# Performance work log

Measured on AMD Instinct MI355X. Metric: run time of the kernel, lower is better.

The kernel has to match this reference:

```python
import jax, jax.numpy as jnp
import numpy as np

D_MODEL, D_K, D_V, H, D_FF = 512, 64, 64, 8, 2048
B, N = 8, 1024
LN_EPS = 1e-5


def _layer_norm(x, g, b):
    mu = jnp.mean(x, axis=-1, keepdims=True)
    var = jnp.mean((x - mu) ** 2, axis=-1, keepdims=True)
    return (x - mu) * jax.lax.rsqrt(var + LN_EPS) * g + b


def setup_inputs() -> dict:
    key = jax.random.key(0)
    ks = jax.random.split(key, 16)
    s = 0.02
    return {
        "queries": jax.random.normal(ks[0], (B, N, D_MODEL), jnp.float32),
        "keys": jax.random.normal(ks[1], (B, N, D_MODEL), jnp.float32),
        "values": jax.random.normal(ks[2], (B, N, D_MODEL), jnp.float32),
        "relative_geometry_weights": jax.random.uniform(ks[3], (B, H, N, N), jnp.float32),
        "pos": jax.random.normal(ks[4], (B, N, D_MODEL), jnp.float32),
        "Wq": jax.random.normal(ks[5], (D_MODEL, H * D_K), jnp.float32) * s,
        "bq": jnp.zeros((H * D_K,), jnp.float32),
        "Wk": jax.random.normal(ks[6], (D_MODEL, H * D_K), jnp.float32) * s,
        "bk": jnp.zeros((H * D_K,), jnp.float32),
        "Wv": jax.random.normal(ks[7], (D_MODEL, H * D_V), jnp.float32) * s,
        "bv": jnp.zeros((H * D_V,), jnp.float32),
        "Wo": jax.random.normal(ks[8], (H * D_V, D_MODEL), jnp.float32) * s,
        "bo": jnp.zeros((D_MODEL,), jnp.float32),
        "ln1_g": jnp.ones((D_MODEL,), jnp.float32),
        "ln1_b": jnp.zeros((D_MODEL,), jnp.float32),
        "W1": jax.random.normal(ks[9], (D_MODEL, D_FF), jnp.float32) * s,
        "b1": jnp.zeros((D_FF,), jnp.float32),
        "W2": jax.random.normal(ks[10], (D_FF, D_MODEL), jnp.float32) * s,
        "b2": jnp.zeros((D_MODEL,), jnp.float32),
        "ln2_g": jnp.ones((D_MODEL,), jnp.float32),
        "ln2_b": jnp.zeros((D_MODEL,), jnp.float32),
    }


def reference(queries, keys, values, relative_geometry_weights, pos,
              Wq, bq, Wk, bk, Wv, bv, Wo, bo, ln1_g, ln1_b,
              W1, b1, W2, b2, ln2_g, ln2_b):
    b, n, _ = queries.shape
    # positional injection on q/k only
    q_in = queries + pos
    k_in = keys + pos
    # projections -> [b, h, n, d]
    q = (q_in @ Wq + bq).reshape(b, n, H, D_K).transpose(0, 2, 1, 3)
    k = (k_in @ Wk + bk).reshape(b, n, H, D_K).transpose(0, 2, 1, 3)
    v = (values @ Wv + bv).reshape(b, n, H, D_V).transpose(0, 2, 1, 3)
    # scaled dot-product scores with geometry bias: log(clamp(w_g)) + scores
    att = jnp.einsum('bhqd,bhkd->bhqk', q, k) / jnp.sqrt(jnp.float32(D_K))
    w_mn = jnp.log(jnp.clip(relative_geometry_weights, 1e-6, None)) + att
    w_mn = jax.nn.softmax(w_mn, axis=-1)
    out = jnp.einsum('bhqk,bhkd->bhqd', w_mn, v)  # [b,h,n,d_v]
    out = out.transpose(0, 2, 1, 3).reshape(b, n, H * D_V) @ Wo + bo
    # residual + layernorm (dropout is identity in eval)
    att_out = _layer_norm(queries + out, ln1_g, ln1_b)
    # position-wise FFN with residual + layernorm
    ff = jax.nn.relu(att_out @ W1 + b1) @ W2 + b2
    return _layer_norm(att_out + ff, ln2_g, ln2_b)
```

## Files before the change

### kernel.cpp

```cpp
#include <hip/hip_runtime.h>
#include <hip/hip_bf16.h>
#include <stdint.h>

#define B_   8
#define N_   1024
#define DM   512
#define H_   8
#define DFF  2048
#define ROWS (B_ * N_)
#define QKV_LD (3 * DM)
#define LOG2E 1.4426950408889634f
#define SCL  (0.125f * LOG2E)

typedef __bf16 bf16x8 __attribute__((ext_vector_type(8)));
typedef float  f32x4  __attribute__((ext_vector_type(4)));

__device__ __forceinline__ void gld_lds16(const void* g, void* l) {
  __builtin_amdgcn_global_load_lds((__attribute__((address_space(1))) void*)g,
                                   (__attribute__((address_space(3))) void*)l, 16, 0, 0);
}

__device__ __forceinline__ unsigned short bfb(float x) {
  __bf16 h = (__bf16)x;
  unsigned short u;
  __builtin_memcpy(&u, &h, 2);
  return u;
}

__global__ __launch_bounds__(256) void prep_and_wt(
    const float* __restrict__ q, const float* __restrict__ k,
    const float* __restrict__ v, const float* __restrict__ pos,
    __bf16* __restrict__ xq, __bf16* __restrict__ xk, __bf16* __restrict__ xv,
    const float* __restrict__ Wq, const float* __restrict__ Wk,
    const float* __restrict__ Wv, const float* __restrict__ Wo,
    const float* __restrict__ W1, const float* __restrict__ W2,
    __bf16* __restrict__ WqkvT, __bf16* __restrict__ WoT,
    __bf16* __restrict__ W1T, __bf16* __restrict__ W2T) {
  __shared__ float tl[32][33];
  if (blockIdx.x < 4096) {
    int i = blockIdx.x * 256 + threadIdx.x;
    float4 pv = ((const float4*)pos)[i];
    float4 qv = ((const float4*)q)[i];
    float4 kv = ((const float4*)k)[i];
    float4 vv = ((const float4*)v)[i];
    ushort4 o;
    o.x = bfb(qv.x + pv.x); o.y = bfb(qv.y + pv.y); o.z = bfb(qv.z + pv.z); o.w = bfb(qv.w + pv.w);
    ((ushort4*)xq)[i] = o;
    o.x = bfb(kv.x + pv.x); o.y = bfb(kv.y + pv.y); o.z = bfb(kv.z + pv.z); o.w = bfb(kv.w + pv.w);
    ((ushort4*)xk)[i] = o;
    o.x = bfb(vv.x); o.y = bfb(vv.y); o.z = bfb(vv.z); o.w = bfb(vv.w);
    ((ushort4*)xv)[i] = o;
    return;
  }
  int idx = blockIdx.x - 4096;
  const float* src; __bf16* dst; int K, N, t;
  if (idx < 768) {
    src = idx < 256 ? Wq : (idx < 512 ? Wk : Wv);
    dst = WqkvT + (size_t)(idx >> 8) * 512 * 512;
    K = 512; N = 512; t = idx & 255;
  } else if (idx < 1024) { src = Wo; dst = WoT;  K = 512;  N = 512;  t = idx - 768; }
  else if (idx < 2048)   { src = W1; dst = W1T;  K = 512;  N = 2048; t = idx - 1024; }
  else                   { src = W2; dst = W2T;  K = 2048; N = 512;  t = idx - 2048; }
  int tiles_n = N >> 5;
  int tn = t & (tiles_n - 1), tk = t / tiles_n;
  int n0 = tn * 32, k0 = tk * 32;
  int x = threadIdx.x & 31, y4 = threadIdx.x >> 5;
  #pragma unroll
  for (int j = y4; j < 32; j += 8) tl[j][x] = src[(size_t)(k0 + j) * N + n0 + x];
  __syncthreads();
  #pragma unroll
  for (int j = y4; j < 32; j += 8)
    dst[(size_t)(n0 + j) * K + k0 + x] = (__bf16)tl[x][j];
}

template <int EPI, int BN>
__global__ __launch_bounds__(256, 2) void gemm_bt(
    const __bf16* __restrict__ A0, const __bf16* __restrict__ A1, const __bf16* __restrict__ A2,
    const __bf16* __restrict__ BT,
    const float* __restrict__ bias0, const float* __restrict__ bias1, const float* __restrict__ bias2,
    void* __restrict__ Cp, __bf16* __restrict__ Vtp, int M, int N, int K, int nsplit) {
  constexpr int NFR = BN / 32;
  constexpr int WCW = BN / 2;
  constexpr int BI  = BN / 32;
  __shared__ __align__(16) __bf16 As[2][128 * 64];
  __shared__ __align__(16) __bf16 Bs[2][BN * 64];
  int tid = threadIdx.x, lane = tid & 63;
  int wave = tid >> 6;
  int wr = (wave >> 1) * 64, wc = (wave & 1) * WCW;

  int gx = N / BN;
  int nwg = gridDim.x;
  int cpx = nwg >> 3;
  int swz = (blockIdx.x & 7) * cpx + (blockIdx.x >> 3);
  int bx = swz % gx, by = swz / gx;
  int row0 = by << 7, col0 = bx * BN;

  int asel = col0 / nsplit;
  const __bf16* A = asel == 0 ? A0 : (asel == 1 ? A1 : A2);
  const float* bias = asel == 0 ? bias0 : (asel == 1 ? bias1 : bias2);

  f32x4 acc[4][NFR] = {};

#define GSTAGE(BUF, KT)                                                        \
  { _Pragma("unroll")                                                          \
    for (int i = 0; i < 4; ++i) {                                              \
      int t = i * 256 + tid;                                                   \
      int r = t >> 3, cS = (t & 7) ^ (r & 7);                                  \
      gld_lds16(A + (size_t)(row0 + r) * K + (KT) + cS * 8, As[BUF] + t * 8);  \
    }                                                                          \
    _Pragma("unroll")                                                          \
    for (int i = 0; i < BI; ++i) {                                             \
      int t = i * 256 + tid;                                                   \
      int r = t >> 3, cS = (t & 7) ^ (r & 7);                                  \
      gld_lds16(BT + (size_t)(col0 + r) * K + (KT) + cS * 8, Bs[BUF] + t * 8); \
    } }

#define GCOMP(BUF)                                                             \
  { const __bf16* Asc = As[BUF];                                               \
    const __bf16* Bsc = Bs[BUF];                                               \
    _Pragma("unroll")                                                          \
    for (int ks = 0; ks < 2; ++ks) {                                           \
      bf16x8 af[4], bfr[NFR];                                                  \
      _Pragma("unroll")                                                        \
      for (int m = 0; m < 4; ++m) {                                            \
        int r = wr + m * 16 + (lane & 15);                                     \
        int c = (ks * 4 + (lane >> 4)) ^ (r & 7);                              \
        af[m] = *(const bf16x8*)(Asc + r * 64 + c * 8);                        \
      }                                                                        \
      _Pragma("unroll")                                                        \
      for (int n = 0; n < NFR; ++n) {                                          \
        int r = wc + n * 16 + (lane & 15);                                     \
        int c = (ks * 4 + (lane >> 4)) ^ (r & 7);                              \
        bfr[n] = *(const bf16x8*)(Bsc + r * 64 + c * 8);                       \
      }                                                                        \
      _Pragma("unroll")                                                        \
      for (int m = 0; m < 4; ++m)                                              \
        _Pragma("unroll")                                                      \
        for (int n = 0; n < NFR; ++n)                                          \
          acc[m][n] = __builtin_amdgcn_mfma_f32_16x16x32_bf16(af[m], bfr[n], acc[m][n], 0, 0, 0); \
    } }

  GSTAGE(0, 0)
  int cur = 0;
  for (int kt = 64; kt < K; kt += 64) {
    GSTAGE(cur ^ 1, kt)
    if constexpr (BN == 128) asm volatile("s_waitcnt vmcnt(8)" ::: "memory");
    else                     asm volatile("s_waitcnt vmcnt(6)" ::: "memory");
    __builtin_amdgcn_s_barrier();
    __builtin_amdgcn_sched_barrier(0);
    GCOMP(cur)
    __builtin_amdgcn_s_barrier();
    cur ^= 1;
  }
  asm volatile("s_waitcnt vmcnt(0)" ::: "memory");
  __builtin_amdgcn_s_barrier();
  __builtin_amdgcn_sched_barrier(0);
  GCOMP(cur)
#undef GSTAGE
#undef GCOMP

  int rb = row0 + wr + ((lane >> 4) << 2);
  int cb = col0 + wc + (lane & 15);
  if (EPI == 3 && asel == 2) {
    int bb = row0 >> 10;
    #pragma unroll
    for (int n = 0; n < NFR; ++n) {
      int c = cb + n * 16;
      int d = c & 63, hh = (c >> 6) & 7;
      float bv = bias[c % nsplit];
      size_t vbase = ((size_t)((bb * 8 + hh) * 64 + d)) << 10;
      #pragma unroll
      for (int m = 0; m < 4; ++m) {
        int r0 = (rb + m * 16) & 1023;
        ushort4 pk;
        pk.x = bfb(acc[m][n][0] + bv);
        pk.y = bfb(acc[m][n][1] + bv);
        pk.z = bfb(acc[m][n][2] + bv);
        pk.w = bfb(acc[m][n][3] + bv);
        *(ushort4*)((__bf16*)Vtp + vbase + r0) = pk;
      }
    }
    return;
  }
  #pragma unroll
  for (int n = 0; n < NFR; ++n) {
    int c = cb + n * 16;
    float bv = bias[c % nsplit];
    #pragma unroll
    for (int m = 0; m < 4; ++m) {
      #pragma unroll
      for (int j = 0; j < 4; ++j) {
        int r = rb + m * 16 + j;
        float v = acc[m][n][j] + bv;
        if (EPI == 1) v = fmaxf(v, 0.f);
        if (EPI == 2) ((float*)Cp)[(size_t)r * N + c] = v;
        else          ((__bf16*)Cp)[(size_t)r * N + c] = (__bf16)v;
      }
    }
  }
}

__global__ __launch_bounds__(256, 4) void attn_kernel(
    const __bf16* __restrict__ QKV, const __bf16* __restrict__ Vt,
    const float* __restrict__ rgw, __bf16* __restrict__ O) {
  __shared__ __align__(16) __bf16 QsPs[64 * 64];
  __shared__ __align__(16) __bf16 Ks[2][64 * 64];
  __shared__ __align__(16) __bf16 Vs[2][64 * 64];

  int tid = threadIdx.x, lane = tid & 63, wave = tid >> 6;
  int flat = (blockIdx.x & 7) * 128 + (blockIdx.x >> 3);
  int qt = flat & 15, h = (flat >> 4) & 7, b = flat >> 7;
  int q0 = qt * 64;
  const int g = lane >> 4, u = lane & 15;

  const float* rgw_p = rgw +
      ((size_t)(b * H_ + h) * N_ + (size_t)(q0 + wave * 16 + u)) * N_ + g * 4;

#define STAGE_KV(BUF, KT)                                                      \
  {                                                                            \
    _Pragma("unroll")                                                          \
    for (int i = 0; i < 2; ++i) {                                              \
      int t = i * 256 + tid;                                                   \
      int r = t >> 3, cS = (t & 7) ^ (r & 7);                                  \
      gld_lds16(QKV + (size_t)(b * N_ + (KT) + r) * QKV_LD + DM + h * 64 + cS * 8, Ks[BUF] + t * 8); \
      gld_lds16(Vt + (size_t)((b * H_ + h) * 64 + r) * N_ + (KT) + cS * 8, Vs[BUF] + t * 8);         \
    }                                                                          \
  }
#define RPF(W, T)                                                              \
  {                                                                            \
    _Pragma("unroll")                                                          \
    for (int n = 0; n < 4; ++n)                                                \
      W[n] = __builtin_nontemporal_load((const f32x4*)(rgw_p + (size_t)(T) * 64 + n * 16)); \
  }

  #pragma unroll
  for (int i = 0; i < 2; ++i) {
    int t = i * 256 + tid;
    int r = t >> 3, cS = (t & 7) ^ (r & 7);
    gld_lds16(QKV + (size_t)(b * N_ + q0 + r) * QKV_LD + h * 64 + cS * 8, QsPs + t * 8);
  }
  STAGE_KV(0, 0)
  __builtin_amdgcn_sched_barrier(0);
  f32x4 wA[4], wB[4];
  RPF(wA, 0) RPF(wB, 1)
  __builtin_amdgcn_sched_barrier(0);

  float l = 0.f;
  f32x4 oacc[4] = {};
  bf16x8 qf[2];
  __bf16* pw = &QsPs[wave * 16 * 64];
  const int wrow = wave * 16 + u;
  union Pk { __bf16 h4[4]; unsigned long long q; };

#define PHASE(T16, WAITSTR, DOSTAGE, DORPF, WCON)                              \
  {                                                                            \
    asm volatile(WAITSTR ::: "memory");                                        \
    __builtin_amdgcn_s_barrier();                                              \
    if (DOSTAGE) { STAGE_KV(((T16) + 1) & 1, ((T16) + 1) * 64) }               \
    __builtin_amdgcn_sched_barrier(0);                                         \
    if ((T16) == 0) {                                                          \
      _Pragma("unroll")                                                        \
      for (int ks = 0; ks < 2; ++ks) {                                         \
        int c = (ks * 4 + g) ^ (wrow & 7);                                     \
        qf[ks] = *(const bf16x8*)(QsPs + wrow * 64 + c * 8);                   \
      }                                                                        \
    }                                                                          \
    f32x4 s[4] = {};                                                           \
    __builtin_amdgcn_s_setprio(1);                                             \
    _Pragma("unroll")                                                          \
    for (int ks = 0; ks < 2; ++ks) {                                           \
      _Pragma("unroll")                                                        \
      for (int n = 0; n < 4; ++n) {                                            \
        int r = n * 16 + u;                                                    \
        int c = (ks * 4 + g) ^ (r & 7);                                        \
        bf16x8 kf = *(const bf16x8*)(Ks[(T16) & 1] + r * 64 + c * 8);          \
        s[n] = __builtin_amdgcn_mfma_f32_16x16x32_bf16(kf, qf[ks], s[n], 0, 0, 0); \
      }                                                                        \
    }                                                                          \
    __builtin_amdgcn_s_setprio(0);                                             \
    if ((T16) == 0) __builtin_amdgcn_s_barrier();   \
    _Pragma("unroll")                                                          \
    for (int n = 0; n < 4; ++n) {                                              \
      Pk pk;                                                                   \
      _Pragma("unroll")                                                        \
      for (int j = 0; j < 4; ++j) {                                            \
        float pv = fmaxf(WCON[n][j], 1e-6f) * exp2f(s[n][j] * SCL);            \
        l += pv;                                                               \
        pk.h4[j] = (__bf16)pv;                                                 \
      }                                                                        \
      int bcol = 2 * n + (g >> 1);                                             \
      *(unsigned long long*)(pw + u * 64 + ((bcol ^ (u & 7)) << 3) + ((g & 1) << 2)) = pk.q; \
    }                                                                          \
    __builtin_amdgcn_sched_barrier(0);                                         \
    if (DORPF) { RPF(WCON, (T16) + 2) }                                        \
    __builtin_amdgcn_sched_barrier(0);                                         \
    __builtin_amdgcn_s_setprio(1);                                             \
    _Pragma("unroll")                                                          \
    for (int ks = 0; ks < 2; ++ks) {                                           \
      int cp = (ks * 4 + g) ^ (u & 7);                                         \
      bf16x8 pa = *(const bf16x8*)(pw + u * 64 + cp * 8);                      \
      _Pragma("unroll")                                                        \
      for (int n = 0; n < 4; ++n) {                                            \
        int r = n * 16 + u;                                                    \
        int c = (ks * 4 + g) ^ (r & 7);                                        \
        bf16x8 vb = *(const bf16x8*)(Vs[(T16) & 1] + r * 64 + c * 8);          \
        oacc[n] = __builtin_amdgcn_mfma_f32_16x16x32_bf16(pa, vb, oacc[n], 0, 0, 0); \
      }                                                                        \
    }                                                                          \
    __builtin_amdgcn_s_setprio(0);                                             \
  }

  PHASE(0,  "s_waitcnt vmcnt(8)", 1, 1, wA)
  PHASE(1,  "s_waitcnt vmcnt(4)", 1, 1, wB)
  PHASE(2,  "s_waitcnt vmcnt(4)", 1, 1, wA)
  PHASE(3,  "s_waitcnt vmcnt(4)", 1, 1, wB)
  PHASE(4,  "s_waitcnt vmcnt(4)", 1, 1, wA)
  PHASE(5,  "s_waitcnt vmcnt(4)", 1, 1, wB)
  PHASE(6,  "s_waitcnt vmcnt(4)", 1, 1, wA)
  PHASE(7,  "s_waitcnt vmcnt(4)", 1, 1, wB)
  PHASE(8,  "s_waitcnt vmcnt(4)", 1, 1, wA)
  PHASE(9,  "s_waitcnt vmcnt(4)", 1, 1, wB)
  PHASE(10, "s_waitcnt vmcnt(4)", 1, 1, wA)
  PHASE(11, "s_waitcnt vmcnt(4)", 1, 1, wB)
  PHASE(12, "s_waitcnt vmcnt(4)", 1, 1, wA)
  PHASE(13, "s_waitcnt vmcnt(4)", 1, 1, wB)
  PHASE(14, "s_waitcnt vmcnt(4)", 1, 0, wA)
  PHASE(15, "s_waitcnt vmcnt(0)", 0, 0, wB)
#undef PHASE
#undef STAGE_KV
#undef RPF

  l += __shfl_xor(l, 16);
  l += __shfl_xor(l, 32);
  float linv[4];
  #pragma unroll
  for (int j = 0; j < 4; ++j)
    linv[j] = 1.f / __shfl(l, (lane & 48) | (g * 4 + j));

  int orow = b * N_ + q0 + wave * 16 + g * 4;
  int ocol = h * 64 + u;
  #pragma unroll
  for (int j = 0; j < 4; ++j)
    #pragma unroll
    for (int n = 0; n < 4; ++n)
      O[(size_t)(orow + j) * DM + ocol + n * 16] = (__bf16)(oacc[n][j] * linv[j]);
}

template <int WRITE_BF, int X2BF>
__global__ __launch_bounds__(256) void ln_kernel(
    const float* __restrict__ x1, const void* __restrict__ x2v,
    const float* __restrict__ gw, const float* __restrict__ bw,
    float* __restrict__ outf, __bf16* __restrict__ outb) {
  __shared__ float red[8];
  int row = blockIdx.x, t = threadIdx.x;
  size_t base = (size_t)row * DM;
  float2 a = ((const float2*)(x1 + base))[t];
  float b0, b1;
  if (X2BF) {
    unsigned p = ((const unsigned*)x2v)[base / 2 + t];
    union { unsigned u; float f; } c0, c1;
    c0.u = p << 16; c1.u = p & 0xffff0000u;
    b0 = c0.f; b1 = c1.f;
  } else {
    float2 bb = ((const float2*)x2v)[base / 2 + t];
    b0 = bb.x; b1 = bb.y;
  }
  float v0 = a.x + b0, v1 = a.y + b1;
  float s = v0 + v1, s2 = v0 * v0 + v1 * v1;
  #pragma unroll
  for (int o = 32; o; o >>= 1) { s += __shfl_xor(s, o); s2 += __shfl_xor(s2, o); }
  int wave = t >> 6;
  if ((t & 63) == 0) { red[wave] = s; red[4 + wave] = s2; }
  __syncthreads();
  s = red[0] + red[1] + red[2] + red[3];
  s2 = red[4] + red[5] + red[6] + red[7];
  float mu = s * (1.f / DM);
  float var = s2 * (1.f / DM) - mu * mu;
  float rstd = rsqrtf(var + 1e-5f);
  float y0 = (v0 - mu) * rstd * gw[2 * t] + bw[2 * t];
  float y1 = (v1 - mu) * rstd * gw[2 * t + 1] + bw[2 * t + 1];
  float2 r; r.x = y0; r.y = y1;
  ((float2*)(outf + base))[t] = r;
  if (WRITE_BF) {
    ushort2 h; h.x = bfb(y0); h.y = bfb(y1);
    ((ushort2*)(outb + base))[t] = h;
  }
}

extern "C" void kernel_launch(void* const* d_in, const int* in_sizes, int n_in,
                              void* d_out, int out_size, void* d_ws, size_t ws_size,
                              hipStream_t stream) {
  const float* queries = (const float*)d_in[0];
  const float* keys    = (const float*)d_in[1];
  const float* values  = (const float*)d_in[2];
  const float* rgw     = (const float*)d_in[3];
  const float* pos     = (const float*)d_in[4];
  const float* Wq = (const float*)d_in[5];
  const float* bq = (const float*)d_in[6];
  const float* Wk = (const float*)d_in[7];
  const float* bk = (const float*)d_in[8];
  const float* Wv = (const float*)d_in[9];
  const float* bv = (const float*)d_in[10];
  const float* Wo = (const float*)d_in[11];
  const float* bo = (const float*)d_in[12];
  const float* ln1g = (const float*)d_in[13];
  const float* ln1b = (const float*)d_in[14];
  const float* W1 = (const float*)d_in[15];
  const float* b1 = (const float*)d_in[16];
  const float* W2 = (const float*)d_in[17];
  const float* b2 = (const float*)d_in[18];
  const float* ln2g = (const float*)d_in[19];
  const float* ln2b = (const float*)d_in[20];
  float* out = (float*)d_out;

  char* ws = (char*)d_ws;
  const size_t SZX = (size_t)ROWS * DM * 2;
  __bf16* Xq    = (__bf16*)(ws);
  __bf16* Xk    = (__bf16*)(ws + SZX);
  __bf16* Xv    = (__bf16*)(ws + 2 * SZX);
  __bf16* WqkvT = (__bf16*)(ws + 3 * SZX);
  __bf16* WoT   = (__bf16*)(ws + 3 * SZX + 1572864);
  __bf16* W1T   = (__bf16*)(ws + 3 * SZX + 2097152);
  __bf16* W2T   = (__bf16*)(ws + 3 * SZX + 4194304);
  __bf16* QKV   = (__bf16*)(ws + 3 * SZX + 6291456);
  __bf16* Vt    = (__bf16*)(ws + 3 * SZX + 6291456 + 3 * SZX);
  __bf16* Oat   = (__bf16*)(ws + 3 * SZX + 6291456 + 4 * SZX);
  __bf16* attprojb = Xq;
  __bf16* attoutb  = Xv;
  float*  attoutf  = (float*)QKV;
  __bf16* ff2b     = Vt;
  __bf16* ff1      = (__bf16*)(ws + 3 * SZX + 6291456 + 5 * SZX);

  prep_and_wt<<<4096 + 3072, 256, 0, stream>>>(
      queries, keys, values, pos, Xq, Xk, Xv,
      Wq, Wk, Wv, Wo, W1, W2, WqkvT, WoT, W1T, W2T);

  gemm_bt<3, 128><<<(ROWS / 128) * (QKV_LD / 128), 256, 0, stream>>>(
      Xq, Xk, Xv, WqkvT, bq, bk, bv, QKV, Vt, ROWS, QKV_LD, DM, DM);

  attn_kernel<<<B_ * H_ * (N_ / 64), 256, 0, stream>>>(QKV, Vt, rgw, Oat);

  gemm_bt<0, 64><<<(ROWS / 128) * (DM / 64), 256, 0, stream>>>(
      Oat, Oat, Oat, WoT, bo, bo, bo, attprojb, nullptr, ROWS, DM, DM, DM);

  ln_kernel<1, 1><<<ROWS, 256, 0, stream>>>(queries, attprojb, ln1g, ln1b, attoutf, attoutb);

  gemm_bt<1, 128><<<(ROWS / 128) * (DFF / 128), 256, 0, stream>>>(
      attoutb, attoutb, attoutb, W1T, b1, b1, b1, ff1, nullptr, ROWS, DFF, DM, DFF);

  gemm_bt<0, 64><<<(ROWS / 128) * (DM / 64), 256, 0, stream>>>(
      ff1, ff1, ff1, W2T, b2, b2, b2, ff2b, nullptr, ROWS, DM, DFF, DM);

  ln_kernel<0, 1><<<ROWS, 256, 0, stream>>>(attoutf, ff2b, ln2g, ln2b, out, nullptr);
}
```

Baseline: 209.8 us.

## Prefetch geometry weights in 128-column pairs and retune attention pipeline

Changes the attention kernel's geometry-weight prefetch from per-tile 64-column loads to 128-column loads covering two KV tiles. The loads are issued earlier in each even phase, and the vmcnt waits are restructured around the new schedule. It also swaps nontemporal loads for regular loads and lowers the launch-bounds occupancy hint from 4 to 3 to make room for the doubled register buffers (16 f32x4 instead of 8). The aim is deeper, longer-lived prefetch that hides the latency of the large rgw stream. The cost is more register pressure, fewer waves per CU, and a full vmcnt(0) drain every other phase.

```diff
diff --git a/kernel.cpp b/kernel.cpp
--- a/kernel.cpp
+++ b/kernel.cpp
@@ -200,7 +200,7 @@
   }
 }
 
-__global__ __launch_bounds__(256, 4) void attn_kernel(
+__global__ __launch_bounds__(256, 3) void attn_kernel(
     const __bf16* __restrict__ QKV, const __bf16* __restrict__ Vt,
     const float* __restrict__ rgw, __bf16* __restrict__ O) {
   __shared__ __align__(16) __bf16 QsPs[64 * 64];
@@ -226,11 +226,11 @@
       gld_lds16(Vt + (size_t)((b * H_ + h) * 64 + r) * N_ + (KT) + cS * 8, Vs[BUF] + t * 8);         \
     }                                                                          \
   }
-#define RPF(W, T)                                                              \
+#define RPF8(W, PQ)                                                            \
   {                                                                            \
     _Pragma("unroll")                                                          \
-    for (int n = 0; n < 4; ++n)                                                \
-      W[n] = __builtin_nontemporal_load((const f32x4*)(rgw_p + (size_t)(T) * 64 + n * 16)); \
+    for (int n = 0; n < 8; ++n)                                                \
+      W[n] = *(const f32x4*)(rgw_p + (size_t)(PQ) * 128 + n * 16);             \
   }
 
   #pragma unroll
@@ -241,8 +241,8 @@
   }
   STAGE_KV(0, 0)
   __builtin_amdgcn_sched_barrier(0);
-  f32x4 wA[4], wB[4];
-  RPF(wA, 0) RPF(wB, 1)
+  f32x4 wE[8], wO[8];
+  RPF8(wE, 0)
   __builtin_amdgcn_sched_barrier(0);
 
   float l = 0.f;
@@ -252,12 +252,14 @@
   const int wrow = wave * 16 + u;
   union Pk { __bf16 h4[4]; unsigned long long q; };
 
-#define PHASE(T16, WAITSTR, DOSTAGE, DORPF, WCON)                              \
+#define PHASE(T16, WAITSTR, DOSTAGE, DORPF, WCON, WOFF, WPF, PQ)               \
   {                                                                            \
     asm volatile(WAITSTR ::: "memory");                                        \
     __builtin_amdgcn_s_barrier();                                              \
     if (DOSTAGE) { STAGE_KV(((T16) + 1) & 1, ((T16) + 1) * 64) }               \
     __builtin_amdgcn_sched_barrier(0);                                         \
+    if (DORPF) { RPF8(WPF, PQ) }                                               \
+    __builtin_amdgcn_sched_barrier(0);                                         \
     if ((T16) == 0) {                                                          \
       _Pragma("unroll")                                                        \
       for (int ks = 0; ks < 2; ++ks) {                                         \
@@ -284,16 +286,13 @@
       Pk pk;                                                                   \
       _Pragma("unroll")                                                        \
       for (int j = 0; j < 4; ++j) {                                            \
-        float pv = fmaxf(WCON[n][j], 1e-6f) * exp2f(s[n][j] * SCL);            \
+        float pv = fmaxf(WCON[(WOFF) + n][j], 1e-6f) * exp2f(s[n][j] * SCL);   \
         l += pv;                                                               \
         pk.h4[j] = (__bf16)pv;                                                 \
       }                                                                        \
       int bcol = 2 * n + (g >> 1);                                             \
       *(unsigned long long*)(pw + u * 64 + ((bcol ^ (u & 7)) << 3) + ((g & 1) << 2)) = pk.q; \
     }                                                                          \
-    __builtin_amdgcn_sched_barrier(0);                                         \
-    if (DORPF) { RPF(WCON, (T16) + 2) }                                        \
-    __builtin_amdgcn_sched_barrier(0);                                         \
     __builtin_amdgcn_s_setprio(1);                                             \
     _Pragma("unroll")                                                          \
     for (int ks = 0; ks < 2; ++ks) {                                           \
@@ -310,25 +309,25 @@
     __builtin_amdgcn_s_setprio(0);                                             \
   }
 
-  PHASE(0,  "s_waitcnt vmcnt(8)", 1, 1, wA)
-  PHASE(1,  "s_waitcnt vmcnt(4)", 1, 1, wB)
-  PHASE(2,  "s_waitcnt vmcnt(4)", 1, 1, wA)
-  PHASE(3,  "s_waitcnt vmcnt(4)", 1, 1, wB)
-  PHASE(4,  "s_waitcnt vmcnt(4)", 1, 1, wA)
-  PHASE(5,  "s_waitcnt vmcnt(4)", 1, 1, wB)
-  PHASE(6,  "s_waitcnt vmcnt(4)", 1, 1, wA)
-  PHASE(7,  "s_waitcnt vmcnt(4)", 1, 1, wB)
-  PHASE(8,  "s_waitcnt vmcnt(4)", 1, 1, wA)
-  PHASE(9,  "s_waitcnt vmcnt(4)", 1, 1, wB)
-  PHASE(10, "s_waitcnt vmcnt(4)", 1, 1, wA)
-  PHASE(11, "s_waitcnt vmcnt(4)", 1, 1, wB)
-  PHASE(12, "s_waitcnt vmcnt(4)", 1, 1, wA)
-  PHASE(13, "s_waitcnt vmcnt(4)", 1, 1, wB)
-  PHASE(14, "s_waitcnt vmcnt(4)", 1, 0, wA)
-  PHASE(15, "s_waitcnt vmcnt(0)", 0, 0, wB)
+  PHASE(0,  "s_waitcnt vmcnt(0)", 1, 1, wE, 0, wO, 1)
+  PHASE(1,  "s_waitcnt vmcnt(8)", 1, 0, wE, 4, wO, 0)
+  PHASE(2,  "s_waitcnt vmcnt(0)", 1, 1, wO, 0, wE, 2)
+  PHASE(3,  "s_waitcnt vmcnt(8)", 1, 0, wO, 4, wE, 0)
+  PHASE(4,  "s_waitcnt vmcnt(0)", 1, 1, wE, 0, wO, 3)
+  PHASE(5,  "s_waitcnt vmcnt(8)", 1, 0, wE, 4, wO, 0)
+  PHASE(6,  "s_waitcnt vmcnt(0)", 1, 1, wO, 0, wE, 4)
+  PHASE(7,  "s_waitcnt vmcnt(8)", 1, 0, wO, 4, wE, 0)
+  PHASE(8,  "s_waitcnt vmcnt(0)", 1, 1, wE, 0, wO, 5)
+  PHASE(9,  "s_waitcnt vmcnt(8)", 1, 0, wE, 4, wO, 0)
+  PHASE(10, "s_waitcnt vmcnt(0)", 1, 1, wO, 0, wE, 6)
+  PHASE(11, "s_waitcnt vmcnt(8)", 1, 0, wO, 4, wE, 0)
+  PHASE(12, "s_waitcnt vmcnt(0)", 1, 1, wE, 0, wO, 7)
+  PHASE(13, "s_waitcnt vmcnt(8)", 1, 0, wE, 4, wO, 0)
+  PHASE(14, "s_waitcnt vmcnt(0)", 1, 0, wO, 0, wE, 0)
+  PHASE(15, "s_waitcnt vmcnt(0)", 0, 0, wO, 4, wE, 0)
 #undef PHASE
 #undef STAGE_KV
-#undef RPF
+#undef RPF8
 
   l += __shfl_xor(l, 16);
   l += __shfl_xor(l, 32);
```

After: 227.4 us. 1.08x slower.
